# Optimization experiments

Measured on AMD Instinct MI355X. Metric: run time of the kernel, lower is better.

Reference implementation:

```python
import jax, jax.numpy as jnp
import numpy as np

LATENT = 64
HEADS = 4
N_A, N_B = 1024, 1024


def setup_inputs() -> dict:
    key = jax.random.key(0)
    ks = jax.random.split(key, 10)
    L = LATENT
    return {
        "rho_real": jax.random.normal(ks[0], (N_A, N_B), dtype=jnp.float32),
        "rho_imag": jax.random.normal(ks[1], (N_A, N_B), dtype=jnp.float32),
        "l_A": jax.random.randint(ks[2], (N_A,), 0, 3),
        "l_B": jax.random.randint(ks[3], (N_B,), 0, 3),
        "Z_A": 6,
        "Z_B": 8,
        # block_encoder: Linear(2, 64) -> SiLU -> Linear(64, latent_dim)
        "W1": jax.random.normal(ks[4], (64, 2), dtype=jnp.float32) * 0.5,
        "b1": jnp.zeros((64,), dtype=jnp.float32),
        "W2": jax.random.normal(ks[5], (L, 64), dtype=jnp.float32) * 0.1,
        "b2": jnp.zeros((L,), dtype=jnp.float32),
        # learned pooling query (1, latent_dim)
        "query": jax.random.normal(ks[6], (1, L), dtype=jnp.float32),
        # nn.MultiheadAttention packed in-projection and out-projection
        "in_proj_w": jax.random.normal(ks[7], (3 * L, L), dtype=jnp.float32) * 0.1,
        "in_proj_b": jnp.zeros((3 * L,), dtype=jnp.float32),
        "out_proj_w": jax.random.normal(ks[8], (L, L), dtype=jnp.float32) * 0.1,
        "out_proj_b": jnp.zeros((L,), dtype=jnp.float32),
    }


def reference(rho_real, rho_imag, l_A, l_B, Z_A, Z_B,
              W1, b1, W2, b2, query, in_proj_w, in_proj_b,
              out_proj_w, out_proj_b):
    L = query.shape[-1]
    H = HEADS
    hd = L // H
    # Batched equivalent of the per-(i,j) loop: all n_A*n_B elements at once.
    x = jnp.stack([rho_real.reshape(-1), rho_imag.reshape(-1)], axis=-1)  # [N, 2]
    h = jax.nn.silu(x @ W1.T + b1) @ W2.T + b2                            # [N, L]
    # MultiheadAttention with single query (batch=1, tgt_len=1, src_len=N)
    Wq, Wk, Wv = in_proj_w[:L], in_proj_w[L:2 * L], in_proj_w[2 * L:]
    bq, bk, bv = in_proj_b[:L], in_proj_b[L:2 * L], in_proj_b[2 * L:]
    q = (query @ Wq.T + bq).reshape(H, hd)        # [H, hd]
    k = (h @ Wk.T + bk).reshape(-1, H, hd)        # [N, H, hd]
    v = (h @ Wv.T + bv).reshape(-1, H, hd)        # [N, H, hd]
    scale = 1.0 / jnp.sqrt(jnp.asarray(hd, dtype=x.dtype))
    scores = jnp.einsum('hd,nhd->hn', q, k) * scale   # [H, N]
    attn = jax.nn.softmax(scores, axis=-1)
    pooled = jnp.einsum('hn,nhd->hd', attn, v).reshape(L)  # [L]
    return pooled @ out_proj_w.T + out_proj_b             # [latent_dim]
```

## Files before the change

kernel.cpp:

```cpp
#include <hip/hip_runtime.h>


#define LOG2E 1.44269504088896340736f
#define NLN2  (-0.69314718055994530942f)

#if __has_builtin(__builtin_amdgcn_exp2f)
#define EXP2(x) __builtin_amdgcn_exp2f(x)
#else
#define EXP2(x) exp2f(x)
#endif
#if __has_builtin(__builtin_amdgcn_rcpf)
#define RCP(x) __builtin_amdgcn_rcpf(x)
#else
#define RCP(x) (1.0f / (x))
#endif

#define LDS_WAIT() asm volatile("s_waitcnt lgkmcnt(0)" ::: "memory")

#define WS_C4   0
#define WS_G4   256
#define WS_D    512
#define WS_ACC  768
#define NSLOT      16
#define SLOTSTRIDE 272

#define NPTS       (1024 * 1024)
#define K1_BLOCKS  2048
#define K1_THREADS 128
#define WAVES_TOTAL (K1_BLOCKS * 2)
#define GROUPS_PER_WAVE ((NPTS / 64) / WAVES_TOTAL)

__device__ __forceinline__ unsigned short to_bf16(float x) {
    return (unsigned short)((__float_as_uint(x) + 0x8000u) >> 16);
}

__global__ void setup_kernel(const float* __restrict__ W1, const float* __restrict__ b1,
                             const float* __restrict__ W2, const float* __restrict__ b2,
                             const float* __restrict__ query,
                             const float* __restrict__ ipw, const float* __restrict__ ipb,
                             float* __restrict__ ws)
{
    __shared__ float qv[64], qs[64], as4[4][64];
    const int t = threadIdx.x;
    const int b = blockIdx.x;

    for (int i = b * 64 + t; i < NSLOT * SLOTSTRIDE; i += 64 * 64)
        ws[WS_ACC + i] = 0.0f;

    qv[t] = query[t];
    __syncthreads();

    {
        float a = ipb[t];
        #pragma unroll
        for (int k = 0; k < 64; ++k) a = fmaf(ipw[t * 64 + k], qv[k], a);
        qs[t] = a;
    }
    __syncthreads();

    #pragma unroll
    for (int h = 0; h < 4; ++h) {
        float a = 0.0f;
        #pragma unroll
        for (int m = 0; m < 16; ++m)
            a = fmaf(ipw[(64 + h * 16 + m) * 64 + t], qs[h * 16 + m], a);
        as4[h][t] = 0.25f * a;
    }
    __syncthreads();

    const float w2 = W2[t * 64 + b];
    float g[4];
    #pragma unroll
    for (int h = 0; h < 4; ++h) {
        float v = as4[h][t] * w2;
        for (int m = 1; m < 64; m <<= 1) v += __shfl_xor(v, m);
        g[h] = v;
    }
    if (t == 0) {
        ws[WS_G4 + b * 4 + 0] = -g[0];
        ws[WS_G4 + b * 4 + 1] = -g[1];
        ws[WS_G4 + b * 4 + 2] = -g[2];
        ws[WS_G4 + b * 4 + 3] = -g[3];
        ws[WS_C4 + b * 4 + 0] = -LOG2E * W1[2 * b];
        ws[WS_C4 + b * 4 + 1] = -LOG2E * W1[2 * b + 1];
        ws[WS_C4 + b * 4 + 2] = -LOG2E * b1[b];
        ws[WS_C4 + b * 4 + 3] = 0.0f;
    }
    if (b == 0 && t < 4) {
        float d = 0.0f;
        #pragma unroll
        for (int c = 0; c < 64; ++c) d += as4[t][c] * b2[c];
        float qb = 0.0f;
        #pragma unroll
        for (int m = 0; m < 16; ++m) qb += qs[t * 16 + m] * ipb[64 + t * 16 + m];
        ws[WS_D + t] = LOG2E * (d + 0.25f * qb);
    }
}

__global__ __launch_bounds__(K1_THREADS) void main_kernel(
        const float* __restrict__ rr, const float* __restrict__ ri,
        const float4* __restrict__ c4g, const float4* __restrict__ g4g,
        const float* __restrict__ dvec, float* __restrict__ accb)
{
    __shared__ unsigned short us[2][64 * 66];
    __shared__ float4 p4s[2][64];

    const int t    = threadIdx.x;
    const int lane = t & 63;
    const int w    = t >> 6;

    const float d0 = dvec[0], d1 = dvec[1], d2 = dvec[2], d3 = dvec[3];

    const int gwave = blockIdx.x * 2 + w;
    float l0 = 0, l1 = 0, l2 = 0, l3 = 0;
    float t0 = 0, t1 = 0, t2 = 0, t3 = 0;
    unsigned short* uw = us[w];

    float rv[GROUPS_PER_WAVE], iv[GROUPS_PER_WAVE];
    #pragma unroll
    for (int it = 0; it < GROUPS_PER_WAVE; ++it) {
        const int idx = (gwave + it * WAVES_TOTAL) * 64 + lane;
        rv[it] = rr[idx];
        iv[it] = ri[idx];
    }

    for (int it = 0; it < GROUPS_PER_WAVE; ++it) {
        const float r  = rv[it];
        const float im = iv[it];

        float s0 = d0, s1 = d1, s2 = d2, s3 = d3;
        #pragma unroll 16
        for (int j = 0; j < 64; ++j) {
            const float4 c  = c4g[j];
            const float4 gg = g4g[j];
            const float zn = fmaf(c.x, r, fmaf(c.y, im, c.z));
            const float e  = EXP2(zn);
            const float rc = RCP(1.0f + e);
            const float ub = zn * rc;
            s0 = fmaf(gg.x, ub, s0);
            s1 = fmaf(gg.y, ub, s1);
            s2 = fmaf(gg.z, ub, s2);
            s3 = fmaf(gg.w, ub, s3);
            uw[j * 66 + lane] = to_bf16(ub);
        }
        const float p0 = EXP2(s0), p1 = EXP2(s1), p2 = EXP2(s2), p3 = EXP2(s3);
        l0 += p0; l1 += p1; l2 += p2; l3 += p3;
        p4s[w][lane] = make_float4(p0, p1, p2, p3);
        LDS_WAIT();

        const unsigned int* urow = (const unsigned int*)(uw + lane * 66);
        #pragma unroll 16
        for (int pp = 0; pp < 32; ++pp) {
            const unsigned int bits = urow[pp];
            const float ulo = __uint_as_float(bits << 16);
            const float uhi = __uint_as_float(bits & 0xFFFF0000u);
            const float4 pa = p4s[w][2 * pp];
            const float4 pb = p4s[w][2 * pp + 1];
            t0 = fmaf(pa.x, ulo, t0); t0 = fmaf(pb.x, uhi, t0);
            t1 = fmaf(pa.y, ulo, t1); t1 = fmaf(pb.y, uhi, t1);
            t2 = fmaf(pa.z, ulo, t2); t2 = fmaf(pb.z, uhi, t2);
            t3 = fmaf(pa.w, ulo, t3); t3 = fmaf(pb.w, uhi, t3);
        }
        LDS_WAIT();
    }

    for (int m = 1; m < 64; m <<= 1) {
        l0 += __shfl_xor(l0, m);
        l1 += __shfl_xor(l1, m);
        l2 += __shfl_xor(l2, m);
        l3 += __shfl_xor(l3, m);
    }

    float* acc = accb + (blockIdx.x & (NSLOT - 1)) * SLOTSTRIDE;
    if (lane == 0) {
        atomicAdd(acc + 0, l0);
        atomicAdd(acc + 1, l1);
        atomicAdd(acc + 2, l2);
        atomicAdd(acc + 3, l3);
    }
    atomicAdd(acc + 4 + 0 * 64 + lane, t0);
    atomicAdd(acc + 4 + 1 * 64 + lane, t1);
    atomicAdd(acc + 4 + 2 * 64 + lane, t2);
    atomicAdd(acc + 4 + 3 * 64 + lane, t3);
}

__global__ void finish_kernel(const float* __restrict__ W2, const float* __restrict__ b2,
                              const float* __restrict__ ipw, const float* __restrict__ ipb,
                              const float* __restrict__ opw, const float* __restrict__ opb,
                              const float* __restrict__ ws, float* __restrict__ out)
{
    __shared__ float red[260];
    __shared__ float sb[256];
    __shared__ float pl[64];
    const int t = threadIdx.x;

    {
        float a = 0.0f;
        for (int s = 0; s < NSLOT; ++s) a += ws[WS_ACC + s * SLOTSTRIDE + t];
        red[t] = a;
        if (t < 4) {
            float a2 = 0.0f;
            for (int s = 0; s < NSLOT; ++s) a2 += ws[WS_ACC + s * SLOTSTRIDE + 256 + t];
            red[256 + t] = a2;
        }
    }
    __syncthreads();

    {
        const int h = t >> 6, j = t & 63;
        const float inv = NLN2 / red[h];
        float a = 0.0f;
        #pragma unroll
        for (int k = 0; k < 64; ++k) a += W2[j * 64 + k] * red[4 + h * 64 + k];
        sb[t] = fmaf(inv, a, b2[j]);
    }
    __syncthreads();

    if (t < 64) {
        const int h = t >> 4;
        float a = ipb[128 + t];
        #pragma unroll
        for (int d = 0; d < 64; ++d) a += ipw[(128 + t) * 64 + d] * sb[h * 64 + d];
        pl[t] = a;
    }
    __syncthreads();

    if (t < 64) {
        float a = opb[t];
        #pragma unroll
        for (int p = 0; p < 64; ++p) a += opw[t * 64 + p] * pl[p];
        out[t] = a;
    }
}

extern "C" void kernel_launch(void* const* d_in, const int* in_sizes, int n_in,
                              void* d_out, int out_size, void* d_ws, size_t ws_size,
                              hipStream_t stream)
{
    const float* rr  = (const float*)d_in[0];
    const float* ri  = (const float*)d_in[1];
    const float* W1  = (const float*)d_in[6];
    const float* b1  = (const float*)d_in[7];
    const float* W2  = (const float*)d_in[8];
    const float* b2  = (const float*)d_in[9];
    const float* qy  = (const float*)d_in[10];
    const float* ipw = (const float*)d_in[11];
    const float* ipb = (const float*)d_in[12];
    const float* opw = (const float*)d_in[13];
    const float* opb = (const float*)d_in[14];
    float* ws  = (float*)d_ws;
    float* out = (float*)d_out;

    setup_kernel<<<64, 64, 0, stream>>>(W1, b1, W2, b2, qy, ipw, ipb, ws);
    main_kernel<<<K1_BLOCKS, K1_THREADS, 0, stream>>>(
        rr, ri,
        (const float4*)(ws + WS_C4), (const float4*)(ws + WS_G4),
        ws + WS_D, ws + WS_ACC);
    finish_kernel<<<1, 256, 0, stream>>>(W2, b2, ipw, ipb, opw, opb, ws, out);
}
```

Baseline: 132.4 us.

## Compute weighted hidden-sum reduction with bf16 MFMA instead of scalar FMAs

Replaces the per-lane scalar FMA loop that accumulates attention-weighted hidden activations with MFMA 16x16x32 bf16 matrix ops. The softmax weights are now stored as bf16 in LDS, padded to 16 heads for the B operand, and the U tile row stride changes to 72 for vector loads. This cuts VALU work and LDS reads per group, but it adds bf16 rounding on the probabilities and wastes part of the MFMA width on padded heads.

```diff
diff --git a/kernel.cpp b/kernel.cpp
--- a/kernel.cpp
+++ b/kernel.cpp
@@ -17,6 +17,9 @@
 
 #define LDS_WAIT() asm volatile("s_waitcnt lgkmcnt(0)" ::: "memory")
 
+typedef __attribute__((ext_vector_type(8))) __bf16 bf16x8;
+typedef __attribute__((ext_vector_type(4))) float  f32x4;
+
 #define WS_C4   0
 #define WS_G4   256
 #define WS_D    512
@@ -29,6 +32,10 @@
 #define K1_THREADS 128
 #define WAVES_TOTAL (K1_BLOCKS * 2)
 #define GROUPS_PER_WAVE ((NPTS / 64) / WAVES_TOTAL)
+
+#define PW_SHORTS  288
+#define UW_SHORTS  (64 * 72)
+#define WAVE_SHORTS (PW_SHORTS + UW_SHORTS)
 
 __device__ __forceinline__ unsigned short to_bf16(float x) {
     return (unsigned short)((__float_as_uint(x) + 0x8000u) >> 16);
@@ -102,19 +109,24 @@
         const float4* __restrict__ c4g, const float4* __restrict__ g4g,
         const float* __restrict__ dvec, float* __restrict__ accb)
 {
-    __shared__ unsigned short us[2][64 * 66];
-    __shared__ float4 p4s[2][64];
+    __shared__ __align__(16) unsigned short lds[2][WAVE_SHORTS];
 
     const int t    = threadIdx.x;
     const int lane = t & 63;
     const int w    = t >> 6;
+    const int m    = lane & 15;
+    const int q    = lane >> 4;
+
+    unsigned short* pw = lds[w];
+    unsigned short* uw = lds[w] + PW_SHORTS;
 
     const float d0 = dvec[0], d1 = dvec[1], d2 = dvec[2], d3 = dvec[3];
 
     const int gwave = blockIdx.x * 2 + w;
     float l0 = 0, l1 = 0, l2 = 0, l3 = 0;
-    float t0 = 0, t1 = 0, t2 = 0, t3 = 0;
-    unsigned short* uw = us[w];
+    f32x4 acc[4];
+    #pragma unroll
+    for (int i = 0; i < 4; ++i) acc[i] = (f32x4){0.f, 0.f, 0.f, 0.f};
 
     float rv[GROUPS_PER_WAVE], iv[GROUPS_PER_WAVE];
     #pragma unroll
@@ -141,47 +153,49 @@
             s1 = fmaf(gg.y, ub, s1);
             s2 = fmaf(gg.z, ub, s2);
             s3 = fmaf(gg.w, ub, s3);
-            uw[j * 66 + lane] = to_bf16(ub);
+            uw[j * 72 + lane] = to_bf16(ub);
         }
         const float p0 = EXP2(s0), p1 = EXP2(s1), p2 = EXP2(s2), p3 = EXP2(s3);
         l0 += p0; l1 += p1; l2 += p2; l3 += p3;
-        p4s[w][lane] = make_float4(p0, p1, p2, p3);
+        pw[0 * 72 + lane] = to_bf16(p0);
+        pw[1 * 72 + lane] = to_bf16(p1);
+        pw[2 * 72 + lane] = to_bf16(p2);
+        pw[3 * 72 + lane] = to_bf16(p3);
         LDS_WAIT();
 
-        const unsigned int* urow = (const unsigned int*)(uw + lane * 66);
-        #pragma unroll 16
-        for (int pp = 0; pp < 32; ++pp) {
-            const unsigned int bits = urow[pp];
-            const float ulo = __uint_as_float(bits << 16);
-            const float uhi = __uint_as_float(bits & 0xFFFF0000u);
-            const float4 pa = p4s[w][2 * pp];
-            const float4 pb = p4s[w][2 * pp + 1];
-            t0 = fmaf(pa.x, ulo, t0); t0 = fmaf(pb.x, uhi, t0);
-            t1 = fmaf(pa.y, ulo, t1); t1 = fmaf(pb.y, uhi, t1);
-            t2 = fmaf(pa.z, ulo, t2); t2 = fmaf(pb.z, uhi, t2);
-            t3 = fmaf(pa.w, ulo, t3); t3 = fmaf(pb.w, uhi, t3);
+        const bf16x8 b0 = *(const bf16x8*)(pw + m * 72 + q * 8);
+        const bf16x8 b1 = *(const bf16x8*)(pw + m * 72 + q * 8 + 32);
+        #pragma unroll
+        for (int tt = 0; tt < 4; ++tt) {
+            const bf16x8 a0 = *(const bf16x8*)(uw + (16 * tt + m) * 72 + q * 8);
+            const bf16x8 a1 = *(const bf16x8*)(uw + (16 * tt + m) * 72 + q * 8 + 32);
+            acc[tt] = __builtin_amdgcn_mfma_f32_16x16x32_bf16(a0, b0, acc[tt], 0, 0, 0);
+            acc[tt] = __builtin_amdgcn_mfma_f32_16x16x32_bf16(a1, b1, acc[tt], 0, 0, 0);
         }
         LDS_WAIT();
     }
 
-    for (int m = 1; m < 64; m <<= 1) {
-        l0 += __shfl_xor(l0, m);
-        l1 += __shfl_xor(l1, m);
-        l2 += __shfl_xor(l2, m);
-        l3 += __shfl_xor(l3, m);
-    }
-
-    float* acc = accb + (blockIdx.x & (NSLOT - 1)) * SLOTSTRIDE;
+    for (int mm = 1; mm < 64; mm <<= 1) {
+        l0 += __shfl_xor(l0, mm);
+        l1 += __shfl_xor(l1, mm);
+        l2 += __shfl_xor(l2, mm);
+        l3 += __shfl_xor(l3, mm);
+    }
+
+    float* accS = accb + (blockIdx.x & (NSLOT - 1)) * SLOTSTRIDE;
     if (lane == 0) {
-        atomicAdd(acc + 0, l0);
-        atomicAdd(acc + 1, l1);
-        atomicAdd(acc + 2, l2);
-        atomicAdd(acc + 3, l3);
-    }
-    atomicAdd(acc + 4 + 0 * 64 + lane, t0);
-    atomicAdd(acc + 4 + 1 * 64 + lane, t1);
-    atomicAdd(acc + 4 + 2 * 64 + lane, t2);
-    atomicAdd(acc + 4 + 3 * 64 + lane, t3);
+        atomicAdd(accS + 0, l0);
+        atomicAdd(accS + 1, l1);
+        atomicAdd(accS + 2, l2);
+        atomicAdd(accS + 3, l3);
+    }
+    if (m < 4) {
+        #pragma unroll
+        for (int tt = 0; tt < 4; ++tt)
+            #pragma unroll
+            for (int reg = 0; reg < 4; ++reg)
+                atomicAdd(accS + 4 + m * 64 + (16 * tt + 4 * q + reg), acc[tt][reg]);
+    }
 }
 
 __global__ void finish_kernel(const float* __restrict__ W2, const float* __restrict__ b2,
```

After: 157.9 us. 1.19x slower.
